# Optimization experiments

Measured on AMD Instinct MI355X. Metric: run time of the kernel, lower is better.

The kernel has to match this reference:

```python
import jax, jax.numpy as jnp
import numpy as np
from jax import lax

CONF_THRESHOLD = 0.01
NMS_THRESHOLD = 0.45
VARIANCES = (0.1, 0.2)
TOPK = 200
NUM_CLASSES = 2


def decode(loc, priors, variances):
    # priors in center-size form (cx, cy, w, h) -> corner form boxes
    centers = priors[:, :2] + loc[:, :2] * variances[0] * priors[:, 2:]
    wh = priors[:, 2:] * jnp.exp(loc[:, 2:] * variances[1])
    return jnp.concatenate([centers - wh * 0.5, centers + wh * 0.5], axis=1)  # [N,4]


def _area(b):
    return (b[..., 2] - b[..., 0]) * (b[..., 3] - b[..., 1])


def _iou_one_vs_all(box, boxes):
    lt = jnp.maximum(box[:2], boxes[:, :2])
    rb = jnp.minimum(box[2:], boxes[:, 2:])
    wh = jnp.clip(rb - lt, 0.0)
    inter = wh[:, 0] * wh[:, 1]
    union = _area(box) + _area(boxes) - inter
    return inter / union


def _per_image(loc, conf, priors):
    boxes = decode(loc, priors, VARIANCES)            # [N,4]
    scores = conf[:, 1]                               # class-1 scores
    masked = jnp.where(scores > CONF_THRESHOLD, scores, 0.0)
    top_scores, top_idx = lax.top_k(masked, TOPK)     # candidates for greedy NMS
    cand_boxes = boxes[top_idx]                       # [K,4]
    valid = top_scores > CONF_THRESHOLD               # below-threshold slots inactive

    def step(active, _):
        s = jnp.where(active, top_scores, -1.0)
        i = jnp.argmax(s)                             # highest-score active candidate
        keep = active[i]
        ious = _iou_one_vs_all(cand_boxes[i], cand_boxes)
        new_active = active & (ious <= NMS_THRESHOLD)
        new_active = new_active.at[i].set(False)
        return new_active, (i, keep)

    _, (idxs, keeps) = lax.scan(step, valid, None, length=TOPK)
    rows = jnp.concatenate([top_scores[idxs][:, None], cand_boxes[idxs]], axis=1)  # [K,5]
    rows = jnp.where(keeps[:, None], rows, 0.0)       # kept boxes are packed at front
    out = jnp.zeros((NUM_CLASSES, TOPK, 5), dtype=loc.dtype).at[1].set(rows)
    return out


def setup_inputs() -> dict:
    key = jax.random.key(0)
    k1, k2, k3 = jax.random.split(key, 3)
    B, N = 32, 200000
    loc_data = jax.random.normal(k1, (B, N, 4), dtype=jnp.float32)
    conf_data = jax.random.uniform(k2, (B, N, 2), dtype=jnp.float32)
    priors = jax.random.uniform(k3, (N, 4), dtype=jnp.float32)  # cx, cy, w, h in (0,1)
    return {"loc_data": loc_data, "conf_data": conf_data, "priors": priors}


def reference(loc_data, conf_data, priors):
    # output: [B, num_classes=2, topk, 5] with (score, x1, y1, x2, y2) per detection
    return jax.vmap(_per_image, in_axes=(0, 0, None))(loc_data, conf_data, priors)
```

## Files before the change

### kernel.cpp

```cpp
#include <hip/hip_runtime.h>

typedef unsigned int u32;
typedef unsigned long long u64;

#define BATCH 32
#define NPRI  200000
#define TOPK  200
#define CAP   4096
#define PRE_BITS 0x3F7F8000u
#define NBLK  64
#define SEGCAP 128
#define NSLICE 4

__device__ __forceinline__ u32 binOf(u64 key) {
  u32 bits = (u32)(key >> 32);
  if (bits < PRE_BITS) return 0u;
  u32 b = (bits - PRE_BITS) >> 6;
  return b > 511u ? 511u : b;
}

__global__ __launch_bounds__(256) void k_cap(const float* __restrict__ conf,
                                             u32* __restrict__ cntA,
                                             u32* __restrict__ cnt1A,
                                             u64* __restrict__ cand) {
  __shared__ u32 lcnt, lc1;
  if (threadIdx.x == 0) { lcnt = 0u; lc1 = 0u; }
  __syncthreads();
  const int img = blockIdx.y;
  const int blk = blockIdx.x;
  const float4* cp = ((const float4*)conf) + (size_t)img * (NPRI/2);
  u64* cd = cand + ((size_t)img * NBLK + blk) * SEGCAP;
  u32 my001 = 0;
  for (int i = blk*256 + threadIdx.x; i < NPRI/2; i += NBLK*256) {
    float4 v = cp[i];
    if (v.y > 0.01f) {
      ++my001;
      u32 bits = __float_as_uint(v.y);
      if (bits >= PRE_BITS) {
        u32 p = atomicAdd(&lcnt, 1u);
        if (p < SEGCAP) cd[p] = ((u64)bits << 32) | (u64)(0xFFFFFFFFu - (u32)(2*i));
      }
    }
    if (v.w > 0.01f) {
      ++my001;
      u32 bits = __float_as_uint(v.w);
      if (bits >= PRE_BITS) {
        u32 p = atomicAdd(&lcnt, 1u);
        if (p < SEGCAP) cd[p] = ((u64)bits << 32) | (u64)(0xFFFFFFFFu - (u32)(2*i+1));
      }
    }
  }
  if (my001) atomicAdd(&lc1, my001);
  __syncthreads();
  if (threadIdx.x == 0) {
    u32 n = lcnt;
    u32 v = (n > SEGCAP) ? (SEGCAP | 0x80000000u) : n;
    cntA[img * NBLK + blk] = v;
    cnt1A[img * NBLK + blk] = lc1;
  }
}

__global__ __launch_bounds__(512) void k_prep(const float* __restrict__ loc,
                                              const float* __restrict__ priors,
                                              const float* __restrict__ conf,
                                              const u32* __restrict__ cntA,
                                              const u32* __restrict__ cnt1A,
                                              const u64* __restrict__ cand,
                                              float4* __restrict__ gbox,
                                              float* __restrict__ gscore,
                                              u32* __restrict__ gmask32) {
  __shared__ u64    lkeys[CAP];
  __shared__ u64    skeys[512];
  __shared__ float4 sbox[TOPK];
  __shared__ float  sarea[TOPK];
  __shared__ float  sscore[TOPK];
  __shared__ u32    suffst[512];
  __shared__ u32    hist[512];
  __shared__ u32    cnt2[512];
  __shared__ u32    pre[NBLK];
  __shared__ u32    ln[NBLK];
  __shared__ u32    s_nc, s_c1, s_flag, s_T, s_ctr;

  const int img = blockIdx.y;
  const int slice = blockIdx.x;
  const int tid = threadIdx.x;
  const u64* gseg = cand + (size_t)img * NBLK * SEGCAP;

  hist[tid] = 0u; cnt2[tid] = 0u; skeys[tid] = 0ull;
  if (tid < 64) {
    u32 v = cntA[img * NBLK + tid];
    u32 n = v & 0x7FFFFFFFu;
    bool ofl = (v >> 31) != 0u;
    u32 c1 = cnt1A[img * NBLK + tid];
    u32 incl = n;
    #pragma unroll
    for (int off = 1; off < 64; off <<= 1) { u32 u = __shfl_up(incl, off); if (tid >= off) incl += u; }
    pre[tid] = incl - n;
    ln[tid] = n;
    u32 tot = __shfl(incl, 63);
    u32 c1s = c1;
    #pragma unroll
    for (int off = 1; off < 64; off <<= 1) c1s += __shfl_xor(c1s, off);
    u64 ob = __ballot(ofl);
    if (tid == 0) { s_nc = tot; s_c1 = c1s; s_flag = (ob != 0ull) ? 1u : 0u; s_T = 0u; s_ctr = 0u; }
  }
  __syncthreads();

  u32 nc = s_nc;
  const bool fb = (s_flag != 0u) || (nc > CAP) || (nc < TOPK && nc < s_c1);

  if (!fb) {
    const int b = tid >> 3, r = tid & 7;
    const u32 nb = ln[b], pb = pre[b];
    const u64* sg = gseg + (size_t)b * SEGCAP;
    for (u32 i = r; i < nb; i += 8) lkeys[pb + i] = sg[i];
  } else {
    u32* ph   = (u32*)lkeys;
    u32* csum = (u32*)skeys;
    for (int t = tid; t < 8192; t += 512) ph[t] = 0u;
    __syncthreads();
    const float4* cp = ((const float4*)conf) + (size_t)img * (NPRI/2);
    for (int i = tid; i < NPRI/2; i += 512) {
      float4 v = cp[i];
      if (v.y > 0.01f) { u32 b = __float_as_uint(v.y) >> 17; atomicAdd(&ph[b >> 1], 1u << ((b & 1) * 16)); }
      if (v.w > 0.01f) { u32 b = __float_as_uint(v.w) >> 17; atomicAdd(&ph[b >> 1], 1u << ((b & 1) * 16)); }
    }
    __syncthreads();
    {
      u32 acc = 0;
      #pragma unroll
      for (int w = 0; w < 16; ++w) { u32 v = ph[tid*16 + w]; acc += (v & 0xFFFFu) + (v >> 16); }
      csum[tid] = acc;
    }
    __syncthreads();
    for (int off = 1; off < 512; off <<= 1) {
      u32 v = (tid + off < 512) ? csum[tid + off] : 0u;
      __syncthreads();
      csum[tid] += v;
      __syncthreads();
    }
    {
      u32 mine = csum[tid], nxt = (tid < 511) ? csum[tid + 1] : 0u;
      if (mine >= TOPK && nxt < TOPK) {
        u32 run = nxt;
        for (int b = 31; b >= 0; --b) {
          u32 bin = tid*32 + b;
          u32 w = ph[bin >> 1];
          run += (bin & 1) ? (w >> 16) : (w & 0xFFFFu);
          if (run >= TOPK) { s_T = bin; break; }
        }
      }
    }
    __syncthreads();
    const u32 T = s_T;
    __syncthreads();
    const float4* cp2 = ((const float4*)conf) + (size_t)img * (NPRI/2);
    for (int i = tid; i < NPRI/2; i += 512) {
      float4 v = cp2[i];
      if (v.y > 0.01f) {
        u32 bits = __float_as_uint(v.y);
        if ((bits >> 17) >= T) { u32 p = atomicAdd(&s_ctr, 1u); if (p < CAP) lkeys[p] = ((u64)bits << 32) | (u64)(0xFFFFFFFFu - (u32)(2*i)); }
      }
      if (v.w > 0.01f) {
        u32 bits = __float_as_uint(v.w);
        if ((bits >> 17) >= T) { u32 p = atomicAdd(&s_ctr, 1u); if (p < CAP) lkeys[p] = ((u64)bits << 32) | (u64)(0xFFFFFFFFu - (u32)(2*i+1)); }
      }
    }
    __syncthreads();
    nc = s_ctr; if (nc > CAP) nc = CAP;
    skeys[tid] = 0ull;
  }
  __syncthreads();

  if (nc <= 512u) {
    if (tid < (int)nc) atomicAdd(&hist[binOf(lkeys[tid])], 1u);
    __syncthreads();
    if (tid < 64) {
      u32 h[8]; u32 s = 0;
      #pragma unroll
      for (int q = 0; q < 8; ++q) { h[q] = hist[tid*8 + q]; s += h[q]; }
      u32 acc = s;
      #pragma unroll
      for (int off = 1; off < 64; off <<= 1) { u32 v = __shfl_down(acc, off); if (tid + off < 64) acc += v; }
      u32 run = acc - s;
      u32 st[8];
      #pragma unroll
      for (int q = 7; q >= 0; --q) { st[q] = run; run += h[q]; }
      #pragma unroll
      for (int q = 0; q < 8; ++q) suffst[tid*8 + q] = st[q];
    }
    __syncthreads();
    u64* tmp = lkeys + 1024;
    if (tid < (int)nc) {
      u64 key = lkeys[tid]; u32 b = binOf(key);
      u32 pos = suffst[b] + atomicAdd(&cnt2[b], 1u);
      tmp[pos] = key;
    }
    __syncthreads();
    if (tid < (int)nc) {
      u64 k = tmp[tid]; u32 b = binOf(k);
      u32 c = hist[b];
      if (c == 1u) skeys[tid] = k;
      else {
        u32 base = suffst[b], r = 0;
        for (u32 q = 0; q < c; ++q) r += (u32)(tmp[base + q] > k);
        skeys[base + r] = k;
      }
    }
  } else {
    u32 ncp = (nc + 7u) & ~7u;
    for (u32 t = tid; t < ncp; t += 512) if (t >= nc) lkeys[t] = 0ull;
    __syncthreads();
    u64 myk[8]; u32 myr[8];
    #pragma unroll
    for (int r = 0; r < 8; ++r) {
      u32 g = (u32)tid + ((u32)r << 9);
      myk[r] = (g < ncp) ? lkeys[g] : 0ull;
      myr[r] = 0u;
    }
    for (u32 j = 0; j < ncp; ++j) {
      u64 kj = lkeys[j];
      #pragma unroll
      for (int r = 0; r < 8; ++r) myr[r] += (u32)(kj > myk[r]);
    }
    #pragma unroll
    for (int r = 0; r < 8; ++r) {
      u32 g = (u32)tid + ((u32)r << 9);
      if (g < nc && myr[r] < 512u) skeys[myr[r]] = myk[r];
    }
  }
  __syncthreads();

  if (tid < TOPK) {
    u64 key = skeys[tid];
    float sc = __uint_as_float((u32)(key >> 32));
    float4 bx = make_float4(0.f, 0.f, 0.f, 0.f);
    if (sc > 0.01f) {
      u32 idx = 0xFFFFFFFFu - (u32)(key & 0xFFFFFFFFull);
      float4 l = ((const float4*)loc)[(size_t)img * NPRI + idx];
      float4 p = ((const float4*)priors)[idx];
      float cx = p.x + (l.x * 0.1f) * p.z;
      float cy = p.y + (l.y * 0.1f) * p.w;
      float w  = p.z * expf(l.z * 0.2f);
      float h  = p.w * expf(l.w * 0.2f);
      bx = make_float4(cx - w * 0.5f, cy - h * 0.5f, cx + w * 0.5f, cy + h * 0.5f);
    } else sc = (sc > 0.01f) ? sc : sc;
    sbox[tid] = bx;
    sarea[tid] = (bx.z - bx.x) * (bx.w - bx.y);
    sscore[tid] = sc;
  }
  __syncthreads();

  {
    const int h = tid >> 8;
    const int row = tid & 255;
    if (row < TOPK) {
      const int j0 = slice * 64 + h * 32;
      int cnt = TOPK - j0; if (cnt > 32) cnt = 32;
      u32 m = 0;
      float4 bi = sbox[row];
      float ai = sarea[row];
      for (int jj = 0; jj < cnt; ++jj) {
        int j = j0 + jj;
        float4 bj = sbox[j];
        float ltx = fmaxf(bi.x, bj.x), lty = fmaxf(bi.y, bj.y);
        float rbx = fminf(bi.z, bj.z), rby = fminf(bi.w, bj.w);
        float w = fmaxf(rbx - ltx, 0.f), hh = fmaxf(rby - lty, 0.f);
        float inter = w * hh;
        float uni = ai + sarea[j] - inter;
        float iou = inter / uni;
        if (!(iou <= 0.45f)) m |= 1u << jj;
      }
      gmask32[((size_t)img * NSLICE * TOPK + (size_t)slice * TOPK + row) * 2 + h] = m;
    }
  }
  if (slice == 0 && tid < TOPK) {
    gbox[(size_t)img * TOPK + tid] = sbox[tid];
    gscore[(size_t)img * TOPK + tid] = sscore[tid];
  }
}

__global__ __launch_bounds__(256) void k_sweep(const float4* __restrict__ gbox,
                                               const float* __restrict__ gscore,
                                               const u64* __restrict__ gmask,
                                               float* __restrict__ out) {
  __shared__ float4 sbx[TOPK];
  __shared__ float  ssc[TOPK];
  __shared__ u64    sact[4];
  const int img = blockIdx.x;
  const int tid = threadIdx.x;
  float* oimg = out + (size_t)img * 2 * TOPK * 5;

  for (int i = tid; i < 2*TOPK*5; i += 256) oimg[i] = 0.0f;
  if (tid < TOPK) {
    sbx[tid] = gbox[(size_t)img * TOPK + tid];
    ssc[tid] = gscore[(size_t)img * TOPK + tid];
  }
  __syncthreads();

  if (tid < 64) {
    const u64* gm = gmask + (size_t)img * NSLICE * TOPK;
    u64 row0[4], row1[4], row2[4], row3[4];
    #pragma unroll
    for (int s = 0; s < 4; ++s) {
      row0[s] = gm[s*TOPK + tid];
      row1[s] = gm[s*TOPK + 64 + tid];
      row2[s] = gm[s*TOPK + 128 + tid];
      row3[s] = (tid < TOPK - 192) ? gm[s*TOPK + 192 + tid] : 0ull;
    }
    bool a0 = ssc[tid] > 0.01f;
    bool a1 = ssc[64 + tid] > 0.01f;
    bool a2 = ssc[128 + tid] > 0.01f;
    bool a3 = (tid < TOPK - 192) ? (ssc[192 + tid] > 0.01f) : false;
    u64 k0 = 0, k1 = 0, k2 = 0, k3 = 0;

    #define SWEEP_SLICE(S, AREG, KREG)                                   \
    {                                                                    \
      u64 aw = __ballot(AREG);                                           \
      while (aw) {                                                       \
        int l = __ffsll((long long)aw) - 1;                              \
        KREG |= 1ull << l;                                               \
        a0 = a0 && !((row0[S] >> l) & 1ull);                             \
        a1 = a1 && !((row1[S] >> l) & 1ull);                             \
        a2 = a2 && !((row2[S] >> l) & 1ull);                             \
        a3 = a3 && !((row3[S] >> l) & 1ull);                             \
        u64 above = (l < 63) ? (~0ull << (l + 1)) : 0ull;                \
        aw = __ballot(AREG) & above;                                     \
      }                                                                  \
    }
    SWEEP_SLICE(0, a0, k0)
    SWEEP_SLICE(1, a1, k1)
    SWEEP_SLICE(2, a2, k2)
    SWEEP_SLICE(3, a3, k3)
    #undef SWEEP_SLICE

    if (tid == 0) { sact[0] = k0; sact[1] = k1; sact[2] = k2; sact[3] = k3; }
  }
  __syncthreads();

  if (tid < TOPK) {
    u64 k0 = sact[0], k1 = sact[1], k2 = sact[2], k3 = sact[3];
    int s = tid >> 6, l = tid & 63;
    u64 w = (s == 0) ? k0 : (s == 1) ? k1 : (s == 2) ? k2 : k3;
    if ((w >> l) & 1ull) {
      u32 rank = __popcll(w & ((1ull << l) - 1ull));
      if (s > 0) rank += __popcll(k0);
      if (s > 1) rank += __popcll(k1);
      if (s > 2) rank += __popcll(k2);
      float4 b = sbx[tid];
      float* row = oimg + ((size_t)TOPK + rank) * 5;
      row[0] = ssc[tid];
      row[1] = b.x; row[2] = b.y; row[3] = b.z; row[4] = b.w;
    }
  }
}

extern "C" void kernel_launch(void* const* d_in, const int* in_sizes, int n_in,
                              void* d_out, int out_size, void* d_ws, size_t ws_size,
                              hipStream_t stream) {
  const float* loc    = (const float*)d_in[0];
  const float* conf   = (const float*)d_in[1];
  const float* priors = (const float*)d_in[2];
  float* out = (float*)d_out;

  char* w = (char*)d_ws;
  u32* cntA  = (u32*)w;                                  w += (size_t)BATCH*NBLK*4;
  u32* cnt1A = (u32*)w;                                  w += (size_t)BATCH*NBLK*4;
  u64* cand  = (u64*)w;                                  w += (size_t)BATCH*NBLK*SEGCAP*8;
  float4* gbox = (float4*)w;                             w += (size_t)BATCH*TOPK*16;
  float* gscore = (float*)w;                             w += (size_t)BATCH*TOPK*4;
  u64* gmask = (u64*)w;

  k_cap  <<<dim3(NBLK, BATCH), 256, 0, stream>>>(conf, cntA, cnt1A, cand);
  k_prep <<<dim3(NSLICE, BATCH), 512, 0, stream>>>(loc, priors, conf, cntA, cnt1A, cand,
                                                   gbox, gscore, (u32*)gmask);
  k_sweep<<<BATCH, 256, 0, stream>>>(gbox, gscore, gmask, out);
}
```

Measured before the change: 41.62 us.

## Double k_prep threads, fuse box decode into sort scatter, split mask rows

k_prep now runs with 1024 threads per block instead of 512. In the fast path, each thread decodes the box for its candidate key before the bin sort and scatters the decoded box and score straight to its sorted position, which removes the separate skeys gather and decode phase. The IoU mask work is split four ways per row into 16-bit chunks instead of two 32-bit chunks, so each thread runs a shorter serial loop. The price is a larger block with more idle threads in the scan phases, and the fallback paths change their strides to match.

After: 42.28 us, median of 2. Within noise of the previous version (+1.6%).

```diff
diff --git a/kernel.cpp b/kernel.cpp
--- a/kernel.cpp
+++ b/kernel.cpp
@@ -2,6 +2,7 @@
 
 typedef unsigned int u32;
 typedef unsigned long long u64;
+typedef unsigned short u16;
 
 #define BATCH 32
 #define NPRI  200000
@@ -60,15 +61,15 @@
   }
 }
 
-__global__ __launch_bounds__(512) void k_prep(const float* __restrict__ loc,
-                                              const float* __restrict__ priors,
-                                              const float* __restrict__ conf,
-                                              const u32* __restrict__ cntA,
-                                              const u32* __restrict__ cnt1A,
-                                              const u64* __restrict__ cand,
-                                              float4* __restrict__ gbox,
-                                              float* __restrict__ gscore,
-                                              u32* __restrict__ gmask32) {
+__global__ __launch_bounds__(1024) void k_prep(const float* __restrict__ loc,
+                                               const float* __restrict__ priors,
+                                               const float* __restrict__ conf,
+                                               const u32* __restrict__ cntA,
+                                               const u32* __restrict__ cnt1A,
+                                               const u64* __restrict__ cand,
+                                               float4* __restrict__ gbox,
+                                               float* __restrict__ gscore,
+                                               u16* __restrict__ gmask16) {
   __shared__ u64    lkeys[CAP];
   __shared__ u64    skeys[512];
   __shared__ float4 sbox[TOPK];
@@ -86,7 +87,13 @@
   const int tid = threadIdx.x;
   const u64* gseg = cand + (size_t)img * NBLK * SEGCAP;
 
-  hist[tid] = 0u; cnt2[tid] = 0u; skeys[tid] = 0ull;
+  if (tid < 512) { hist[tid] = 0u; cnt2[tid] = 0u; skeys[tid] = 0ull; }
+  if (tid < TOPK) {
+    sbox[tid] = make_float4(0.f, 0.f, 0.f, 0.f);
+    sarea[tid] = 0.f;
+    sscore[tid] = 0.f;
+  }
+  if (tid == 0) { s_T = 0u; s_ctr = 0u; }
   if (tid < 64) {
     u32 v = cntA[img * NBLK + tid];
     u32 n = v & 0x7FFFFFFFu;
@@ -102,31 +109,33 @@
     #pragma unroll
     for (int off = 1; off < 64; off <<= 1) c1s += __shfl_xor(c1s, off);
     u64 ob = __ballot(ofl);
-    if (tid == 0) { s_nc = tot; s_c1 = c1s; s_flag = (ob != 0ull) ? 1u : 0u; s_T = 0u; s_ctr = 0u; }
+    if (tid == 0) { s_nc = tot; s_c1 = c1s; s_flag = (ob != 0ull) ? 1u : 0u; }
   }
   __syncthreads();
 
   u32 nc = s_nc;
   const bool fb = (s_flag != 0u) || (nc > CAP) || (nc < TOPK && nc < s_c1);
+  bool generic = fb;
 
   if (!fb) {
-    const int b = tid >> 3, r = tid & 7;
+    const int b = tid >> 4, r = tid & 15;
     const u32 nb = ln[b], pb = pre[b];
     const u64* sg = gseg + (size_t)b * SEGCAP;
-    for (u32 i = r; i < nb; i += 8) lkeys[pb + i] = sg[i];
+    for (u32 i = r; i < nb; i += 16) lkeys[pb + i] = sg[i];
+    if (nc > 512u) generic = true;
   } else {
     u32* ph   = (u32*)lkeys;
     u32* csum = (u32*)skeys;
-    for (int t = tid; t < 8192; t += 512) ph[t] = 0u;
+    for (int t = tid; t < 8192; t += 1024) ph[t] = 0u;
     __syncthreads();
     const float4* cp = ((const float4*)conf) + (size_t)img * (NPRI/2);
-    for (int i = tid; i < NPRI/2; i += 512) {
+    for (int i = tid; i < NPRI/2; i += 1024) {
       float4 v = cp[i];
-      if (v.y > 0.01f) { u32 b = __float_as_uint(v.y) >> 17; atomicAdd(&ph[b >> 1], 1u << ((b & 1) * 16)); }
-      if (v.w > 0.01f) { u32 b = __float_as_uint(v.w) >> 17; atomicAdd(&ph[b >> 1], 1u << ((b & 1) * 16)); }
-    }
-    __syncthreads();
-    {
+      if (v.y > 0.01f) { u32 b = __float_as_uint(v.y) >> 17; atomicAdd(&ph[b >> 1], 1u << ((b & 1)*16)); }
+      if (v.w > 0.01f) { u32 b = __float_as_uint(v.w) >> 17; atomicAdd(&ph[b >> 1], 1u << ((b & 1)*16)); }
+    }
+    __syncthreads();
+    if (tid < 512) {
       u32 acc = 0;
       #pragma unroll
       for (int w = 0; w < 16; ++w) { u32 v = ph[tid*16 + w]; acc += (v & 0xFFFFu) + (v >> 16); }
@@ -134,13 +143,13 @@
     }
     __syncthreads();
     for (int off = 1; off < 512; off <<= 1) {
-      u32 v = (tid + off < 512) ? csum[tid + off] : 0u;
+      u32 v = (tid < 512 && tid + off < 512) ? csum[tid + off] : 0u;
       __syncthreads();
-      csum[tid] += v;
+      if (tid < 512) csum[tid] += v;
       __syncthreads();
     }
-    {
-      u32 mine = csum[tid], nxt = (tid < 511) ? csum[tid + 1] : 0u;
+    if (tid < 512) {
+      u32 mine = csum[tid], nxt = (tid < 511) ? csum[tid+1] : 0u;
       if (mine >= TOPK && nxt < TOPK) {
         u32 run = nxt;
         for (int b = 31; b >= 0; --b) {
@@ -154,110 +163,129 @@
     __syncthreads();
     const u32 T = s_T;
     __syncthreads();
-    const float4* cp2 = ((const float4*)conf) + (size_t)img * (NPRI/2);
-    for (int i = tid; i < NPRI/2; i += 512) {
-      float4 v = cp2[i];
+    for (int i = tid; i < NPRI/2; i += 1024) {
+      float4 v = cp[i];
       if (v.y > 0.01f) {
         u32 bits = __float_as_uint(v.y);
-        if ((bits >> 17) >= T) { u32 p = atomicAdd(&s_ctr, 1u); if (p < CAP) lkeys[p] = ((u64)bits << 32) | (u64)(0xFFFFFFFFu - (u32)(2*i)); }
+        if ((bits>>17) >= T) { u32 p = atomicAdd(&s_ctr,1u); if (p < CAP) lkeys[p] = ((u64)bits<<32)|(u64)(0xFFFFFFFFu-(u32)(2*i)); }
       }
       if (v.w > 0.01f) {
         u32 bits = __float_as_uint(v.w);
-        if ((bits >> 17) >= T) { u32 p = atomicAdd(&s_ctr, 1u); if (p < CAP) lkeys[p] = ((u64)bits << 32) | (u64)(0xFFFFFFFFu - (u32)(2*i+1)); }
+        if ((bits>>17) >= T) { u32 p = atomicAdd(&s_ctr,1u); if (p < CAP) lkeys[p] = ((u64)bits<<32)|(u64)(0xFFFFFFFFu-(u32)(2*i+1)); }
       }
     }
     __syncthreads();
     nc = s_ctr; if (nc > CAP) nc = CAP;
-    skeys[tid] = 0ull;
-  }
-  __syncthreads();
-
-  if (nc <= 512u) {
-    if (tid < (int)nc) atomicAdd(&hist[binOf(lkeys[tid])], 1u);
-    __syncthreads();
-    if (tid < 64) {
-      u32 h[8]; u32 s = 0;
-      #pragma unroll
-      for (int q = 0; q < 8; ++q) { h[q] = hist[tid*8 + q]; s += h[q]; }
-      u32 acc = s;
-      #pragma unroll
-      for (int off = 1; off < 64; off <<= 1) { u32 v = __shfl_down(acc, off); if (tid + off < 64) acc += v; }
-      u32 run = acc - s;
-      u32 st[8];
-      #pragma unroll
-      for (int q = 7; q >= 0; --q) { st[q] = run; run += h[q]; }
-      #pragma unroll
-      for (int q = 0; q < 8; ++q) suffst[tid*8 + q] = st[q];
-    }
-    __syncthreads();
-    u64* tmp = lkeys + 1024;
+    if (tid < 512) skeys[tid] = 0ull;
+  }
+  __syncthreads();
+
+  if (!generic) {
+    u64 mykey = 0; u32 mybin = 0;
+    float4 mybox = make_float4(0.f, 0.f, 0.f, 0.f);
+    float mysc = 0.f;
     if (tid < (int)nc) {
-      u64 key = lkeys[tid]; u32 b = binOf(key);
-      u32 pos = suffst[b] + atomicAdd(&cnt2[b], 1u);
-      tmp[pos] = key;
-    }
-    __syncthreads();
-    if (tid < (int)nc) {
-      u64 k = tmp[tid]; u32 b = binOf(k);
-      u32 c = hist[b];
-      if (c == 1u) skeys[tid] = k;
-      else {
-        u32 base = suffst[b], r = 0;
-        for (u32 q = 0; q < c; ++q) r += (u32)(tmp[base + q] > k);
-        skeys[base + r] = k;
-      }
-    }
-  } else {
-    u32 ncp = (nc + 7u) & ~7u;
-    for (u32 t = tid; t < ncp; t += 512) if (t >= nc) lkeys[t] = 0ull;
-    __syncthreads();
-    u64 myk[8]; u32 myr[8];
-    #pragma unroll
-    for (int r = 0; r < 8; ++r) {
-      u32 g = (u32)tid + ((u32)r << 9);
-      myk[r] = (g < ncp) ? lkeys[g] : 0ull;
-      myr[r] = 0u;
-    }
-    for (u32 j = 0; j < ncp; ++j) {
-      u64 kj = lkeys[j];
-      #pragma unroll
-      for (int r = 0; r < 8; ++r) myr[r] += (u32)(kj > myk[r]);
-    }
-    #pragma unroll
-    for (int r = 0; r < 8; ++r) {
-      u32 g = (u32)tid + ((u32)r << 9);
-      if (g < nc && myr[r] < 512u) skeys[myr[r]] = myk[r];
-    }
-  }
-  __syncthreads();
-
-  if (tid < TOPK) {
-    u64 key = skeys[tid];
-    float sc = __uint_as_float((u32)(key >> 32));
-    float4 bx = make_float4(0.f, 0.f, 0.f, 0.f);
-    if (sc > 0.01f) {
-      u32 idx = 0xFFFFFFFFu - (u32)(key & 0xFFFFFFFFull);
+      mykey = lkeys[tid];
+      mysc = __uint_as_float((u32)(mykey >> 32));
+      mybin = binOf(mykey);
+      atomicAdd(&hist[mybin], 1u);
+      u32 idx = 0xFFFFFFFFu - (u32)(mykey & 0xFFFFFFFFull);
       float4 l = ((const float4*)loc)[(size_t)img * NPRI + idx];
       float4 p = ((const float4*)priors)[idx];
       float cx = p.x + (l.x * 0.1f) * p.z;
       float cy = p.y + (l.y * 0.1f) * p.w;
       float w  = p.z * expf(l.z * 0.2f);
       float h  = p.w * expf(l.w * 0.2f);
-      bx = make_float4(cx - w * 0.5f, cy - h * 0.5f, cx + w * 0.5f, cy + h * 0.5f);
-    } else sc = (sc > 0.01f) ? sc : sc;
-    sbox[tid] = bx;
-    sarea[tid] = (bx.z - bx.x) * (bx.w - bx.y);
-    sscore[tid] = sc;
-  }
-  __syncthreads();
-
-  {
-    const int h = tid >> 8;
-    const int row = tid & 255;
-    if (row < TOPK) {
-      const int j0 = slice * 64 + h * 32;
-      int cnt = TOPK - j0; if (cnt > 32) cnt = 32;
-      u32 m = 0;
+      mybox = make_float4(cx - w*0.5f, cy - h*0.5f, cx + w*0.5f, cy + h*0.5f);
+    }
+    __syncthreads();
+    if (tid < 64) {
+      u32 h[8]; u32 s = 0;
+      #pragma unroll
+      for (int q = 0; q < 8; ++q) { h[q] = hist[tid*8 + q]; s += h[q]; }
+      u32 acc = s;
+      #pragma unroll
+      for (int off = 1; off < 64; off <<= 1) { u32 v = __shfl_down(acc, off); if (tid + off < 64) acc += v; }
+      u32 run = acc - s;
+      u32 st[8];
+      #pragma unroll
+      for (int q = 7; q >= 0; --q) { st[q] = run; run += h[q]; }
+      #pragma unroll
+      for (int q = 0; q < 8; ++q) suffst[tid*8 + q] = st[q];
+    }
+    __syncthreads();
+    u64* tmp = lkeys + 1024;
+    if (tid < (int)nc) tmp[suffst[mybin] + atomicAdd(&cnt2[mybin], 1u)] = mykey;
+    __syncthreads();
+    if (tid < (int)nc) {
+      u32 c = hist[mybin], base = suffst[mybin];
+      u32 pos = base;
+      if (c > 1u) {
+        u32 r2 = 0;
+        for (u32 q = 0; q < c; ++q) r2 += (u32)(tmp[base + q] > mykey);
+        pos = base + r2;
+      }
+      if (pos < TOPK) {
+        sbox[pos] = mybox;
+        sarea[pos] = (mybox.z - mybox.x) * (mybox.w - mybox.y);
+        sscore[pos] = mysc;
+      }
+    }
+  } else {
+    u32 ncp = (nc + 3u) & ~3u;
+    for (u32 t = tid; t < ncp; t += 1024) if (t >= nc) lkeys[t] = 0ull;
+    __syncthreads();
+    u64 myk[4]; u32 myr[4];
+    #pragma unroll
+    for (int r2 = 0; r2 < 4; ++r2) {
+      u32 g = (u32)tid + ((u32)r2 << 10);
+      myk[r2] = (g < ncp) ? lkeys[g] : 0ull;
+      myr[r2] = 0u;
+    }
+    for (u32 j = 0; j < ncp; ++j) {
+      u64 kj = lkeys[j];
+      #pragma unroll
+      for (int r2 = 0; r2 < 4; ++r2) myr[r2] += (u32)(kj > myk[r2]);
+    }
+    #pragma unroll
+    for (int r2 = 0; r2 < 4; ++r2) {
+      u32 g = (u32)tid + ((u32)r2 << 10);
+      if (g < nc && myr[r2] < 512u) skeys[myr[r2]] = myk[r2];
+    }
+    __syncthreads();
+    if (tid < TOPK) {
+      u64 key = skeys[tid];
+      float sc = __uint_as_float((u32)(key >> 32));
+      float4 bx = make_float4(0.f, 0.f, 0.f, 0.f);
+      if (sc > 0.01f) {
+        u32 idx = 0xFFFFFFFFu - (u32)(key & 0xFFFFFFFFull);
+        float4 l = ((const float4*)loc)[(size_t)img * NPRI + idx];
+        float4 p = ((const float4*)priors)[idx];
+        float cx = p.x + (l.x * 0.1f) * p.z;
+        float cy = p.y + (l.y * 0.1f) * p.w;
+        float w  = p.z * expf(l.z * 0.2f);
+        float h  = p.w * expf(l.w * 0.2f);
+        bx = make_float4(cx - w*0.5f, cy - h*0.5f, cx + w*0.5f, cy + h*0.5f);
+      }
+      sbox[tid] = bx;
+      sarea[tid] = (bx.z - bx.x) * (bx.w - bx.y);
+      sscore[tid] = sc;
+    }
+  }
+  __syncthreads();
+
+  if (slice == 0 && tid < TOPK) {
+    gbox[(size_t)img * TOPK + tid] = sbox[tid];
+    gscore[(size_t)img * TOPK + tid] = sscore[tid];
+  }
+
+  if (tid < 4*TOPK) {
+    const int row = tid >> 2;
+    const int q = tid & 3;
+    const int j0 = slice*64 + q*16;
+    int cnt = TOPK - j0; if (cnt > 16) cnt = 16;
+    u32 m = 0;
+    if (cnt > 0) {
       float4 bi = sbox[row];
       float ai = sarea[row];
       for (int jj = 0; jj < cnt; ++jj) {
@@ -271,12 +299,8 @@
         float iou = inter / uni;
         if (!(iou <= 0.45f)) m |= 1u << jj;
       }
-      gmask32[((size_t)img * NSLICE * TOPK + (size_t)slice * TOPK + row) * 2 + h] = m;
-    }
-  }
-  if (slice == 0 && tid < TOPK) {
-    gbox[(size_t)img * TOPK + tid] = sbox[tid];
-    gscore[(size_t)img * TOPK + tid] = sscore[tid];
+    }
+    gmask16[(((size_t)img*NSLICE + slice)*TOPK + row)*4 + q] = (u16)m;
   }
 }
 
@@ -372,7 +396,7 @@
   u64* gmask = (u64*)w;
 
   k_cap  <<<dim3(NBLK, BATCH), 256, 0, stream>>>(conf, cntA, cnt1A, cand);
-  k_prep <<<dim3(NSLICE, BATCH), 512, 0, stream>>>(loc, priors, conf, cntA, cnt1A, cand,
-                                                   gbox, gscore, (u32*)gmask);
+  k_prep <<<dim3(NSLICE, BATCH), 1024, 0, stream>>>(loc, priors, conf, cntA, cnt1A, cand,
+                                                    gbox, gscore, (u16*)gmask);
   k_sweep<<<BATCH, 256, 0, stream>>>(gbox, gscore, gmask, out);
 }
```
